# Optimization experiments

Hardware: AMD Instinct MI355X
Metric: run time of the kernel (lower is better)

The kernel has to match this reference:

```python
import jax, jax.numpy as jnp
import numpy as np

B, N, D, H = 8, 2048, 128, 128  # batch, num_nodes, input_size, hidden_size


def setup_inputs() -> dict:
    key = jax.random.key(0)
    ks = jax.random.split(key, 10)
    s = 1.0 / np.sqrt(H)
    u = lambda k, shape: jax.random.uniform(k, shape, jnp.float32, -s, s)
    return {
        "x": jax.random.normal(ks[0], (B, N, D), jnp.float32),
        "adj_matrix": jax.random.randint(ks[1], (B, N, N), 0, 2, jnp.int32),
        # PyTorch LSTM params, gate order (i, f, g, o); forward + backward dirs
        "w_ih_f": u(ks[2], (4 * H, D)),
        "w_hh_f": u(ks[3], (4 * H, H)),
        "b_ih_f": u(ks[4], (4 * H,)),
        "b_hh_f": u(ks[5], (4 * H,)),
        "w_ih_b": u(ks[6], (4 * H, D)),
        "w_hh_b": u(ks[7], (4 * H, H)),
        "b_ih_b": u(ks[8], (4 * H,)),
        "b_hh_b": u(ks[9], (4 * H,)),
    }


def _lstm_last_h(xp, w_hh):
    # xp: [T, B, 4H] precomputed input projection + biases; returns final h [B, H]
    b = xp.shape[1]
    h0 = jnp.zeros((b, H), xp.dtype)
    c0 = jnp.zeros((b, H), xp.dtype)

    def step(carry, xt):
        h, c = carry
        gates = xt + h @ w_hh.T
        i, f, g, o = jnp.split(gates, 4, axis=-1)
        c = jax.nn.sigmoid(f) * c + jax.nn.sigmoid(i) * jnp.tanh(g)
        h = jax.nn.sigmoid(o) * jnp.tanh(c)
        return (h, c), None

    (hT, _), _ = jax.lax.scan(step, (h0, c0), xp)
    return hT


def reference(x, adj_matrix, w_ih_f, w_hh_f, b_ih_f, b_hh_f, w_ih_b, w_hh_b, b_ih_b, b_hh_b):
    x = x.astype(jnp.float32)
    a = (adj_matrix > 0).astype(jnp.float32)  # [B, N, N]
    # mean over {self} + neighbors: (x_i + sum_j a_ij x_j) / (1 + deg_i)
    deg = a.sum(-1, keepdims=True)
    xa = (x + jnp.einsum('bij,bjd->bid', a, x)) / (1.0 + deg)  # [B, N, D]

    seq = jnp.swapaxes(xa, 0, 1)  # [N, B, D], time-major over nodes
    hT_f = _lstm_last_h(seq @ w_ih_f.T + (b_ih_f + b_hh_f), w_hh_f)
    hT_b = _lstm_last_h(seq[::-1] @ w_ih_b.T + (b_ih_b + b_hh_b), w_hh_b)
    return jnp.concatenate([hT_f, hT_b], axis=-1)  # [B, 2H]
```

## Files before the change

### kernel.cpp

```cpp
#include <hip/hip_runtime.h>
#include <math.h>

#define BB 8
#define NN 2048
#define DD 128
#define HH 128

typedef float f4 __attribute__((ext_vector_type(4)));
typedef __attribute__((ext_vector_type(8))) short s16x8;
typedef __attribute__((ext_vector_type(8))) unsigned short u16x8;

__device__ __forceinline__ float fast_rcp(float x) { return __builtin_amdgcn_rcpf(x); }

__device__ __forceinline__ void bsplit(float x, unsigned short& h, unsigned short& l) {
    unsigned u = __float_as_uint(x);
    unsigned r = u + 0x7FFFu + ((u >> 16) & 1u);
    h = (unsigned short)(r >> 16);
    float xh = __uint_as_float(((unsigned)h) << 16);
    float d = x - xh;
    unsigned u2 = __float_as_uint(d);
    unsigned r2 = u2 + 0x7FFFu + ((u2 >> 16) & 1u);
    l = (unsigned short)(r2 >> 16);
}

__global__ __launch_bounds__(256) void k_xT(const float* __restrict__ x,
                                            unsigned short* __restrict__ xth,
                                            unsigned short* __restrict__ xtl) {
    __shared__ __align__(16) unsigned short th[32][72];
    __shared__ __align__(16) unsigned short tl[32][72];
    const int n0 = blockIdx.x * 64;
    const int d0 = blockIdx.y * 32;
    const int b = blockIdx.z;
    const int tid = threadIdx.x;
    {
        const int nl = tid & 63, dseg = tid >> 6;
        const float* xp = x + ((size_t)b * NN + n0 + nl) * DD + d0 + dseg * 8;
        float4 v0 = *(const float4*)(xp);
        float4 v1 = *(const float4*)(xp + 4);
        const float* vv = (const float*)&v0;
#pragma unroll
        for (int j = 0; j < 4; ++j) {
            unsigned short hh, ll;
            bsplit(vv[j], hh, ll);
            th[dseg * 8 + j][nl] = hh;
            tl[dseg * 8 + j][nl] = ll;
        }
        const float* vw = (const float*)&v1;
#pragma unroll
        for (int j = 0; j < 4; ++j) {
            unsigned short hh, ll;
            bsplit(vw[j], hh, ll);
            th[dseg * 8 + 4 + j][nl] = hh;
            tl[dseg * 8 + 4 + j][nl] = ll;
        }
    }
    __syncthreads();
    {
        const int dl = tid >> 3, nseg = tid & 7;
        u16x8 vh = *(const u16x8*)&th[dl][nseg * 8];
        u16x8 vl = *(const u16x8*)&tl[dl][nseg * 8];
        size_t off = ((size_t)b * DD + d0 + dl) * NN + n0 + nseg * 8;
        *(u16x8*)(xth + off) = vh;
        *(u16x8*)(xtl + off) = vl;
    }
}

__global__ __launch_bounds__(256) void k_agg2(const int* __restrict__ adj,
                                              const unsigned short* __restrict__ xth,
                                              const unsigned short* __restrict__ xtl,
                                              unsigned short* __restrict__ xah,
                                              unsigned short* __restrict__ xal) {
    __shared__ __align__(16) unsigned short Al[64][40];
    __shared__ __align__(16) unsigned short Xh[128][40];
    __shared__ __align__(16) unsigned short Xl[128][40];
    const int b = blockIdx.y;
    const int i0 = blockIdx.x * 64;
    const int tid = threadIdx.x;
    const int wave = tid >> 6, lane = tid & 63;
    const int ar = tid >> 2, aks = (tid & 3) * 8;
    const int xd = tid >> 1, xks = (tid & 1) * 16;
    const int* ap = adj + ((size_t)b * NN + i0 + ar) * NN + aks;
    const unsigned short* hp = xth + ((size_t)b * DD + xd) * NN + xks;
    const unsigned short* lp = xtl + ((size_t)b * DD + xd) * NN + xks;

    f4 acc[8], dacc;
#pragma unroll
    for (int t = 0; t < 8; ++t) acc[t] = {0.f, 0.f, 0.f, 0.f};
    dacc = {0.f, 0.f, 0.f, 0.f};
    const short onebf = (short)0x3F80;
    s16x8 ones = {onebf, onebf, onebf, onebf, onebf, onebf, onebf, onebf};

    int4 a0 = *(const int4*)(ap);
    int4 a1 = *(const int4*)(ap + 4);
    u16x8 h0 = *(const u16x8*)(hp);
    u16x8 h1 = *(const u16x8*)(hp + 8);
    u16x8 l0 = *(const u16x8*)(lp);
    u16x8 l1 = *(const u16x8*)(lp + 8);

    for (int k0 = 0; k0 < NN; k0 += 32) {
        {
            u16x8 w;
            const int* av0 = (const int*)&a0;
            const int* av1 = (const int*)&a1;
            int colb = k0 + aks, myrow = i0 + ar;
#pragma unroll
            for (int j = 0; j < 4; ++j) {
                int c0 = (av0[j] > 0 ? 1 : 0) + (myrow == colb + j ? 1 : 0);
                int c1 = (av1[j] > 0 ? 1 : 0) + (myrow == colb + 4 + j ? 1 : 0);
                w[j] = c0 == 0 ? 0 : (c0 == 1 ? 0x3F80 : 0x4000);
                w[4 + j] = c1 == 0 ? 0 : (c1 == 1 ? 0x3F80 : 0x4000);
            }
            *(u16x8*)&Al[ar][aks] = w;
            *(u16x8*)&Xh[xd][xks] = h0;
            *(u16x8*)&Xh[xd][xks + 8] = h1;
            *(u16x8*)&Xl[xd][xks] = l0;
            *(u16x8*)&Xl[xd][xks + 8] = l1;
        }
        __syncthreads();
        if (k0 + 32 < NN) {
            a0 = *(const int4*)(ap + k0 + 32);
            a1 = *(const int4*)(ap + k0 + 36);
            h0 = *(const u16x8*)(hp + k0 + 32);
            h1 = *(const u16x8*)(hp + k0 + 40);
            l0 = *(const u16x8*)(lp + k0 + 32);
            l1 = *(const u16x8*)(lp + k0 + 40);
        }
        s16x8 afr = *(const s16x8*)&Al[16 * wave + (lane & 15)][(lane >> 4) * 8];
#pragma unroll
        for (int t = 0; t < 8; ++t) {
            s16x8 bh = *(const s16x8*)&Xh[16 * t + (lane & 15)][(lane >> 4) * 8];
            s16x8 bl = *(const s16x8*)&Xl[16 * t + (lane & 15)][(lane >> 4) * 8];
            acc[t] = __builtin_amdgcn_mfma_f32_16x16x32_bf16(afr, bh, acc[t], 0, 0, 0);
            acc[t] = __builtin_amdgcn_mfma_f32_16x16x32_bf16(afr, bl, acc[t], 0, 0, 0);
        }
        dacc = __builtin_amdgcn_mfma_f32_16x16x32_bf16(afr, ones, dacc, 0, 0, 0);
        __syncthreads();
    }
    float inv[4];
#pragma unroll
    for (int r = 0; r < 4; ++r) inv[r] = fast_rcp(dacc[r]);
#pragma unroll
    for (int t = 0; t < 8; ++t)
#pragma unroll
        for (int r = 0; r < 4; ++r) {
            int row = i0 + 16 * wave + (lane >> 4) * 4 + r;
            float v = acc[t][r] * inv[r];
            unsigned short hh, ll;
            bsplit(v, hh, ll);
            size_t base = ((size_t)b * NN + row) * DD + 16 * t + (lane & 15);
            xah[base] = hh;
            xal[base] = ll;
        }
}

__global__ __launch_bounds__(256) void k_proj2(const unsigned short* __restrict__ xah,
                                               const unsigned short* __restrict__ xal,
                                               const float* __restrict__ wif,
                                               const float* __restrict__ wib,
                                               const float* __restrict__ bif,
                                               const float* __restrict__ bhf,
                                               const float* __restrict__ bib,
                                               const float* __restrict__ bhb,
                                               float* __restrict__ xpf,
                                               float* __restrict__ xpb) {
    __shared__ __align__(16) unsigned short Wh[128][132];
    __shared__ __align__(16) unsigned short Wl[128][132];
    const int rr0 = blockIdx.x * 64;
    const int n0 = blockIdx.y * 128;
    const int tid = threadIdx.x;
    const int wave = tid >> 6, lane = tid & 63;
    {
        int g = tid >> 1;
        int d0 = (tid & 1) * 64;
        int gg = n0 + g;
        const float* wsrc = (gg < 512) ? (wif + (size_t)gg * DD) : (wib + (size_t)(gg - 512) * DD);
#pragma unroll
        for (int j = 0; j < 64; j += 4) {
            float4 v = *(const float4*)(wsrc + d0 + j);
            unsigned short hh, ll;
            bsplit(v.x, hh, ll); Wh[g][d0 + j + 0] = hh; Wl[g][d0 + j + 0] = ll;
            bsplit(v.y, hh, ll); Wh[g][d0 + j + 1] = hh; Wl[g][d0 + j + 1] = ll;
            bsplit(v.z, hh, ll); Wh[g][d0 + j + 2] = hh; Wl[g][d0 + j + 2] = ll;
            bsplit(v.w, hh, ll); Wh[g][d0 + j + 3] = hh; Wl[g][d0 + j + 3] = ll;
        }
    }
    __syncthreads();
    const int arow = rr0 + wave * 16 + (lane & 15);
    const unsigned short* ah = xah + (size_t)arow * DD + ((lane >> 4) * 8);
    const unsigned short* al = xal + (size_t)arow * DD + ((lane >> 4) * 8);
    f4 acc[8];
#pragma unroll
    for (int nt = 0; nt < 8; ++nt) acc[nt] = {0.f, 0.f, 0.f, 0.f};
#pragma unroll
    for (int k0 = 0; k0 < DD; k0 += 32) {
        s16x8 afh = *(const s16x8*)(ah + k0);
        s16x8 afl = *(const s16x8*)(al + k0);
#pragma unroll
        for (int nt = 0; nt < 8; ++nt) {
            s16x8 bh = *(const s16x8*)&Wh[nt * 16 + (lane & 15)][k0 + (lane >> 4) * 8];
            s16x8 bl = *(const s16x8*)&Wl[nt * 16 + (lane & 15)][k0 + (lane >> 4) * 8];
            acc[nt] = __builtin_amdgcn_mfma_f32_16x16x32_bf16(afh, bh, acc[nt], 0, 0, 0);
            acc[nt] = __builtin_amdgcn_mfma_f32_16x16x32_bf16(afl, bh, acc[nt], 0, 0, 0);
            acc[nt] = __builtin_amdgcn_mfma_f32_16x16x32_bf16(afh, bl, acc[nt], 0, 0, 0);
        }
    }
#pragma unroll
    for (int nt = 0; nt < 8; ++nt) {
        int gg = n0 + nt * 16 + (lane & 15);
        float bias = (gg < 512) ? (bif[gg] + bhf[gg]) : (bib[gg - 512] + bhb[gg - 512]);
#pragma unroll
        for (int r = 0; r < 4; ++r) {
            int rr = rr0 + wave * 16 + (lane >> 4) * 4 + r;
            int b = rr >> 11, t = rr & 2047;
            float v = acc[nt][r] + bias;
            if (gg < 512) {
                int pp = 4 * (gg & 127) + (gg >> 7);
                xpf[((size_t)t * BB + b) * 512 + pp] = v;
            } else {
                int gb = gg - 512;
                int pp = 4 * (gb & 127) + (gb >> 7);
                xpb[((size_t)(NN - 1 - t) * BB + b) * 512 + pp] = v;
            }
        }
    }
}


#define STRG(x) #x
#define WLD(R0, R3, WOFF, IMM)                                            \
    "global_load_dwordx4 v[" STRG(R0) ":" STRG(R3) "], %[" STRG(WOFF) "], %[whs] offset:" STRG(IMM) "\n\t"
#define PKQ(H0, H1, A0, A1, B0, B1, C0, C1, D0, D1)                                        \
    "v_pk_fma_f32 v[24:25], v[" STRG(A0) ":" STRG(A1) "], v[" STRG(H0) ":" STRG(H1) "], v[24:25]\n\t" \
    "v_pk_fma_f32 v[26:27], v[" STRG(B0) ":" STRG(B1) "], v[" STRG(H0) ":" STRG(H1) "], v[26:27]\n\t" \
    "v_pk_fma_f32 v[28:29], v[" STRG(C0) ":" STRG(C1) "], v[" STRG(H0) ":" STRG(H1) "], v[28:29]\n\t" \
    "v_pk_fma_f32 v[30:31], v[" STRG(D0) ":" STRG(D1) "], v[" STRG(H0) ":" STRG(H1) "], v[30:31]\n\t"
#define PKQ0(H0, H1, A0, A1, B0, B1, C0, C1, D0, D1)                                       \
    "v_pk_mul_f32 v[24:25], v[" STRG(A0) ":" STRG(A1) "], v[" STRG(H0) ":" STRG(H1) "]\n\t" \
    "v_pk_mul_f32 v[26:27], v[" STRG(B0) ":" STRG(B1) "], v[" STRG(H0) ":" STRG(H1) "]\n\t" \
    "v_pk_mul_f32 v[28:29], v[" STRG(C0) ":" STRG(C1) "], v[" STRG(H0) ":" STRG(H1) "]\n\t" \
    "v_pk_mul_f32 v[30:31], v[" STRG(D0) ":" STRG(D1) "], v[" STRG(H0) ":" STRG(H1) "]\n\t"

#define LSTM_BODY(XPD, XPU, RD, WR)                                                        \
    "global_load_dword " XPD ", v21, %[xps]\n\t"                                           \
    "ds_read_b128 v[32:35], " RD "\n\t"                                                    \
    "ds_read_b128 v[36:39], " RD " offset:16\n\t"                                          \
    "ds_read_b128 v[40:43], " RD " offset:32\n\t"                                          \
    "ds_read_b128 v[44:47], " RD " offset:48\n\t"                                          \
    "ds_read_b128 v[48:51], " RD " offset:64\n\t"                                          \
    "ds_read_b128 v[52:55], " RD " offset:80\n\t"                                          \
    "ds_read_b128 v[56:59], " RD " offset:96\n\t"                                          \
    "ds_read_b128 v[60:63], " RD " offset:112\n\t"                                         \
    "v_add_u32 v21, 0x4000, v21\n\t"                                                       \
    "s_waitcnt lgkmcnt(7)\n\t"                                                             \
    PKQ0(32, 33, 64, 65, 96, 97, 128, 129, 160, 161)                                       \
    PKQ(34, 35, 66, 67, 98, 99, 130, 131, 162, 163)                                        \
    "s_waitcnt lgkmcnt(6)\n\t"                                                             \
    PKQ(36, 37, 68, 69, 100, 101, 132, 133, 164, 165)                                      \
    PKQ(38, 39, 70, 71, 102, 103, 134, 135, 166, 167)                                      \
    "s_waitcnt lgkmcnt(5)\n\t"                                                             \
    PKQ(40, 41, 72, 73, 104, 105, 136, 137, 168, 169)                                      \
    PKQ(42, 43, 74, 75, 106, 107, 138, 139, 170, 171)                                      \
    "s_waitcnt lgkmcnt(4)\n\t"                                                             \
    PKQ(44, 45, 76, 77, 108, 109, 140, 141, 172, 173)                                      \
    PKQ(46, 47, 78, 79, 110, 111, 142, 143, 174, 175)                                      \
    "s_waitcnt lgkmcnt(3)\n\t"                                                             \
    PKQ(48, 49, 80, 81, 112, 113, 144, 145, 176, 177)                                      \
    PKQ(50, 51, 82, 83, 114, 115, 146, 147, 178, 179)                                      \
    "s_waitcnt lgkmcnt(2)\n\t"                                                             \
    PKQ(52, 53, 84, 85, 116, 117, 148, 149, 180, 181)                                      \
    PKQ(54, 55, 86, 87, 118, 119, 150, 151, 182, 183)                                      \
    "s_waitcnt lgkmcnt(1)\n\t"                                                             \
    PKQ(56, 57, 88, 89, 120, 121, 152, 153, 184, 185)                                      \
    PKQ(58, 59, 90, 91, 122, 123, 154, 155, 186, 187)                                      \
    "s_waitcnt lgkmcnt(0)\n\t"                                                             \
    PKQ(60, 61, 92, 93, 124, 125, 156, 157, 188, 189)                                      \
    PKQ(62, 63, 94, 95, 126, 127, 158, 159, 190, 191)                                      \
    "v_add_f32 v8, v24, v25\n\t"                                                           \
    "v_add_f32 v9, v26, v27\n\t"                                                           \
    "v_add_f32 v10, v28, v29\n\t"                                                          \
    "v_add_f32 v11, v30, v31\n\t"                                                          \
    "v_mov_b32_dpp v12, v8 quad_perm:[1,0,3,2] row_mask:0xf bank_mask:0xf\n\t"             \
    "v_mov_b32_dpp v13, v9 quad_perm:[1,0,3,2] row_mask:0xf bank_mask:0xf\n\t"             \
    "v_mov_b32_dpp v14, v10 quad_perm:[1,0,3,2] row_mask:0xf bank_mask:0xf\n\t"            \
    "v_mov_b32_dpp v15, v11 quad_perm:[1,0,3,2] row_mask:0xf bank_mask:0xf\n\t"            \
    "v_add_f32 v8, v8, v12\n\t"                                                            \
    "v_add_f32 v9, v9, v13\n\t"                                                            \
    "v_add_f32 v10, v10, v14\n\t"                                                          \
    "v_add_f32 v11, v11, v15\n\t"                                                          \
    "v_mov_b32_dpp v12, v8 quad_perm:[2,3,0,1] row_mask:0xf bank_mask:0xf\n\t"             \
    "v_mov_b32_dpp v13, v9 quad_perm:[2,3,0,1] row_mask:0xf bank_mask:0xf\n\t"             \
    "v_mov_b32_dpp v14, v10 quad_perm:[2,3,0,1] row_mask:0xf bank_mask:0xf\n\t"            \
    "v_mov_b32_dpp v15, v11 quad_perm:[2,3,0,1] row_mask:0xf bank_mask:0xf\n\t"            \
    "v_add_f32 v8, v8, v12\n\t"                                                            \
    "v_add_f32 v9, v9, v13\n\t"                                                            \
    "v_add_f32 v10, v10, v14\n\t"                                                          \
    "v_add_f32 v11, v11, v15\n\t"                                                          \
    "v_mul_f32 v12, %[s0], v8\n\t"                                                         \
    "v_fma_f32 v12, %[s1], v9, v12\n\t"                                                    \
    "v_fma_f32 v12, %[s2], v10, v12\n\t"                                                   \
    "s_waitcnt vmcnt(1)\n\t"                                                               \
    "v_fma_f32 v12, %[s3], v11, v12\n\t"                                                   \
    "v_add_f32 v12, v12, " XPU "\n\t"                                                      \
    "v_mul_f32 v13, %[ml], v12\n\t"                                                        \
    "v_exp_f32 v13, v13\n\t"                                                               \
    "s_nop 1\n\t"                                                                          \
    "v_add_f32 v13, 1.0, v13\n\t"                                                          \
    "v_rcp_f32 v13, v13\n\t"                                                               \
    "s_nop 1\n\t"                                                                          \
    "v_fma_f32 v12, %[Aa], v13, %[Ba]\n\t"                                                 \
    "s_nop 1\n\t"                                                                          \
    "v_mov_b32_dpp v13, v12 quad_perm:[0,0,0,0] row_mask:0xf bank_mask:0xf\n\t"            \
    "v_mov_b32_dpp v14, v12 quad_perm:[2,2,2,2] row_mask:0xf bank_mask:0xf\n\t"            \
    "v_mov_b32_dpp v15, v12 quad_perm:[1,1,1,1] row_mask:0xf bank_mask:0xf\n\t"            \
    "v_mov_b32_dpp v17, v12 quad_perm:[3,3,3,3] row_mask:0xf bank_mask:0xf\n\t"            \
    "v_mul_f32 v13, v13, v14\n\t"                                                          \
    "v_fma_f32 v16, v15, v16, v13\n\t"                                                     \
    "v_mul_f32 v14, 0xc038aa3b, v16\n\t"                                                   \
    "v_exp_f32 v14, v14\n\t"                                                               \
    "s_nop 1\n\t"                                                                          \
    "v_add_f32 v14, 1.0, v14\n\t"                                                          \
    "v_rcp_f32 v14, v14\n\t"                                                               \
    "s_nop 1\n\t"                                                                          \
    "v_fma_f32 v14, 2.0, v14, -1.0\n\t"                                                    \
    "v_mul_f32 v17, v14, v17\n\t"                                                          \
    "ds_write_b32 " WR ", v17\n\t"                                                         \
    "s_waitcnt lgkmcnt(0)\n\t"                                                             \
    "s_barrier\n\t"

__global__ __launch_bounds__(512) void k_lstm(const float* __restrict__ xpf,
                                              const float* __restrict__ xpb,
                                              const float* __restrict__ whf,
                                              const float* __restrict__ whb,
                                              float* __restrict__ out) {
    const int b = blockIdx.x;
    const int dir = blockIdx.y;
    const float* __restrict__ xp = dir ? xpb : xpf;
    const float* __restrict__ wh = dir ? whb : whf;
    const int t = threadIdx.x;
    const int q = t >> 2;
    const int jq = t & 3;

    __shared__ __align__(64) float h_lds[1088];
    for (int i = t; i < 1088; i += 512) h_lds[i] = 0.f;
    __syncthreads();

    unsigned hbase = (unsigned)(uintptr_t)&h_lds[0];
    unsigned rd0 = hbase + 672u * (unsigned)jq;
    unsigned rd1 = rd0 + 2176u;
    unsigned wrE = hbase + 2176u + 544u * (unsigned)jq + ((unsigned)q << 2);
    unsigned wrO = wrE - 2176u;
    unsigned w0 = ((0u * 128u + (unsigned)q) * 128u + (unsigned)jq * 32u) * 4u;
    unsigned w1 = ((1u * 128u + (unsigned)q) * 128u + (unsigned)jq * 32u) * 4u;
    unsigned w2 = ((2u * 128u + (unsigned)q) * 128u + (unsigned)jq * 32u) * 4u;
    unsigned w3 = ((3u * 128u + (unsigned)q) * 128u + (unsigned)jq * 32u) * 4u;
    unsigned xoff = (unsigned)(b * 512 + t) * 4u + 16384u;
    float xp0v = xp[(size_t)b * 512 + t];
    float s0 = (jq == 0) ? 1.f : 0.f;
    float s1 = (jq == 1) ? 1.f : 0.f;
    float s2 = (jq == 2) ? 1.f : 0.f;
    float s3 = (jq == 3) ? 1.f : 0.f;
    float mlv = (jq == 2) ? -2.8853900817779268f : -1.4426950408889634f;
    float Aav = (jq == 2) ? 2.f : 1.f;
    float Bav = (jq == 2) ? -1.f : 0.f;
    float h_out;

    asm volatile(
        "v_mov_b32 v16, 0\n\t"
        "s_movk_i32 s20, 0x400\n\t"
        "v_mov_b32 v19, %[x0]\n\t"
        "v_mov_b32 v21, %[xo]\n\t"
        "v_mov_b32 v22, %[rdb]\n\t"
        "v_mov_b32 v18, %[rdb2]\n\t"
        "v_mov_b32 v23, %[wrb]\n\t"
        "v_mov_b32 v192, %[wrb2]\n\t"
        WLD(64, 67, w0, 0) WLD(68, 71, w0, 16) WLD(72, 75, w0, 32) WLD(76, 79, w0, 48)
        WLD(80, 83, w0, 64) WLD(84, 87, w0, 80) WLD(88, 91, w0, 96) WLD(92, 95, w0, 112)
        WLD(96, 99, w1, 0) WLD(100, 103, w1, 16) WLD(104, 107, w1, 32) WLD(108, 111, w1, 48)
        WLD(112, 115, w1, 64) WLD(116, 119, w1, 80) WLD(120, 123, w1, 96) WLD(124, 127, w1, 112)
        WLD(128, 131, w2, 0) WLD(132, 135, w2, 16) WLD(136, 139, w2, 32) WLD(140, 143, w2, 48)
        WLD(144, 147, w2, 64) WLD(148, 151, w2, 80) WLD(152, 155, w2, 96) WLD(156, 159, w2, 112)
        WLD(160, 163, w3, 0) WLD(164, 167, w3, 16) WLD(168, 171, w3, 32) WLD(172, 175, w3, 48)
        WLD(176, 179, w3, 64) WLD(180, 183, w3, 80) WLD(184, 187, w3, 96) WLD(188, 191, w3, 112)
        "s_waitcnt vmcnt(0)\n\t"
        "LSTM_TOP%=:\n\t"
        LSTM_BODY("v20", "v19", "v22", "v23")
        LSTM_BODY("v19", "v20", "v18", "v192")
        "s_sub_u32 s20, s20, 1\n\t"
        "s_cmp_lg_u32 s20, 0\n\t"
        "s_cbranch_scc1 LSTM_TOP%=\n\t"
        "v_mov_b32 %[ho], v17\n\t"
        : [ho] "=v"(h_out)
        : [w0] "v"(w0), [w1] "v"(w1), [w2] "v"(w2), [w3] "v"(w3),
          [whs] "s"(wh), [xps] "s"(xp),
          [xo] "v"(xoff), [rdb] "v"(rd0), [rdb2] "v"(rd1),
          [wrb] "v"(wrE), [wrb2] "v"(wrO), [x0] "v"(xp0v),
          [s0] "v"(s0), [s1] "v"(s1), [s2] "v"(s2), [s3] "v"(s3),
          [ml] "v"(mlv), [Aa] "v"(Aav), [Ba] "v"(Bav)
        : "memory", "vcc", "scc", "s20",
          "v8", "v9", "v10", "v11", "v12", "v13", "v14", "v15", "v16", "v17",
          "v18", "v19", "v20", "v21", "v22", "v23", "v24", "v25", "v26", "v27",
          "v28", "v29", "v30", "v31", "v32", "v33", "v34", "v35", "v36", "v37",
          "v38", "v39", "v40", "v41", "v42", "v43", "v44", "v45", "v46", "v47",
          "v48", "v49", "v50", "v51", "v52", "v53", "v54", "v55", "v56", "v57",
          "v58", "v59", "v60", "v61", "v62", "v63", "v64", "v65", "v66", "v67",
          "v68", "v69", "v70", "v71", "v72", "v73", "v74", "v75", "v76", "v77",
          "v78", "v79", "v80", "v81", "v82", "v83", "v84", "v85", "v86", "v87",
          "v88", "v89", "v90", "v91", "v92", "v93", "v94", "v95", "v96", "v97",
          "v98", "v99", "v100", "v101", "v102", "v103", "v104", "v105", "v106", "v107",
          "v108", "v109", "v110", "v111", "v112", "v113", "v114", "v115", "v116", "v117",
          "v118", "v119", "v120", "v121", "v122", "v123", "v124", "v125", "v126", "v127",
          "v128", "v129", "v130", "v131", "v132", "v133", "v134", "v135", "v136", "v137",
          "v138", "v139", "v140", "v141", "v142", "v143", "v144", "v145", "v146", "v147",
          "v148", "v149", "v150", "v151", "v152", "v153", "v154", "v155", "v156", "v157",
          "v158", "v159", "v160", "v161", "v162", "v163", "v164", "v165", "v166", "v167",
          "v168", "v169", "v170", "v171", "v172", "v173", "v174", "v175", "v176", "v177",
          "v178", "v179", "v180", "v181", "v182", "v183", "v184", "v185", "v186", "v187",
          "v188", "v189", "v190", "v191", "v192");

    if (jq == 0) out[(size_t)b * 256 + dir * HH + q] = h_out;
}

extern "C" void kernel_launch(void* const* d_in, const int* in_sizes, int n_in,
                              void* d_out, int out_size, void* d_ws, size_t ws_size,
                              hipStream_t stream) {
    const float* x = (const float*)d_in[0];
    const int* adj = (const int*)d_in[1];
    const float* wif = (const float*)d_in[2];
    const float* whf = (const float*)d_in[3];
    const float* bif = (const float*)d_in[4];
    const float* bhf = (const float*)d_in[5];
    const float* wib = (const float*)d_in[6];
    const float* whb = (const float*)d_in[7];
    const float* bib = (const float*)d_in[8];
    const float* bhb = (const float*)d_in[9];
    float* out = (float*)d_out;

    float* xpf = (float*)d_ws;
    float* xpb = xpf + (size_t)NN * BB * 512;
    unsigned short* xah = (unsigned short*)(xpb + (size_t)NN * BB * 512);
    unsigned short* xal = xah + (size_t)BB * NN * DD;
    unsigned short* xth = (unsigned short*)xpf;
    unsigned short* xtl = xth + (size_t)BB * DD * NN;

    k_xT<<<dim3(NN / 64, DD / 32, BB), 256, 0, stream>>>(x, xth, xtl);
    k_agg2<<<dim3(NN / 64, BB), 256, 0, stream>>>(adj, xth, xtl, xah, xal);
    k_proj2<<<dim3((NN * BB) / 64, 1024 / 128), 256, 0, stream>>>(xah, xal, wif, wib, bif, bhf,
                                                                  bib, bhb, xpf, xpb);
    k_lstm<<<dim3(BB, 2), 512, 0, stream>>>(xpf, xpb, whf, whb, out);
}
```

Measured before the change: 1.209 ms.

## Split aggregation tile across eight waves by row and column halves

```diff
diff --git a/kernel.cpp b/kernel.cpp
--- a/kernel.cpp
+++ b/kernel.cpp
@@ -9,6 +9,7 @@
 typedef float f4 __attribute__((ext_vector_type(4)));
 typedef __attribute__((ext_vector_type(8))) short s16x8;
 typedef __attribute__((ext_vector_type(8))) unsigned short u16x8;
+typedef __attribute__((ext_vector_type(4))) unsigned short u16x4;
 
 __device__ __forceinline__ float fast_rcp(float x) { return __builtin_amdgcn_rcpf(x); }
 
@@ -65,7 +66,7 @@
     }
 }
 
-__global__ __launch_bounds__(256) void k_agg2(const int* __restrict__ adj,
+__global__ __launch_bounds__(512) void k_agg2(const int* __restrict__ adj,
                                               const unsigned short* __restrict__ xth,
                                               const unsigned short* __restrict__ xtl,
                                               unsigned short* __restrict__ xah,
@@ -77,59 +78,50 @@
     const int i0 = blockIdx.x * 64;
     const int tid = threadIdx.x;
     const int wave = tid >> 6, lane = tid & 63;
-    const int ar = tid >> 2, aks = (tid & 3) * 8;
-    const int xd = tid >> 1, xks = (tid & 1) * 16;
-    const int* ap = adj + ((size_t)b * NN + i0 + ar) * NN + aks;
+    const int rt = wave >> 1;
+    const int colh = wave & 1;
+    const int ar = tid >> 3, ak = (tid & 7) * 4;
+    const int xd = tid >> 2, xks = (tid & 3) * 8;
+    const int* ap = adj + ((size_t)b * NN + i0 + ar) * NN + ak;
     const unsigned short* hp = xth + ((size_t)b * DD + xd) * NN + xks;
     const unsigned short* lp = xtl + ((size_t)b * DD + xd) * NN + xks;
 
-    f4 acc[8], dacc;
-#pragma unroll
-    for (int t = 0; t < 8; ++t) acc[t] = {0.f, 0.f, 0.f, 0.f};
+    f4 acc[4], dacc;
+#pragma unroll
+    for (int t = 0; t < 4; ++t) acc[t] = {0.f, 0.f, 0.f, 0.f};
     dacc = {0.f, 0.f, 0.f, 0.f};
     const short onebf = (short)0x3F80;
     s16x8 ones = {onebf, onebf, onebf, onebf, onebf, onebf, onebf, onebf};
 
     int4 a0 = *(const int4*)(ap);
-    int4 a1 = *(const int4*)(ap + 4);
     u16x8 h0 = *(const u16x8*)(hp);
-    u16x8 h1 = *(const u16x8*)(hp + 8);
     u16x8 l0 = *(const u16x8*)(lp);
-    u16x8 l1 = *(const u16x8*)(lp + 8);
 
     for (int k0 = 0; k0 < NN; k0 += 32) {
         {
-            u16x8 w;
-            const int* av0 = (const int*)&a0;
-            const int* av1 = (const int*)&a1;
-            int colb = k0 + aks, myrow = i0 + ar;
+            u16x4 w;
+            const int* av = (const int*)&a0;
+            int colb = k0 + ak, myrow = i0 + ar;
 #pragma unroll
             for (int j = 0; j < 4; ++j) {
-                int c0 = (av0[j] > 0 ? 1 : 0) + (myrow == colb + j ? 1 : 0);
-                int c1 = (av1[j] > 0 ? 1 : 0) + (myrow == colb + 4 + j ? 1 : 0);
-                w[j] = c0 == 0 ? 0 : (c0 == 1 ? 0x3F80 : 0x4000);
-                w[4 + j] = c1 == 0 ? 0 : (c1 == 1 ? 0x3F80 : 0x4000);
+                int c = (av[j] > 0 ? 1 : 0) + (myrow == colb + j ? 1 : 0);
+                w[j] = c == 0 ? 0 : (c == 1 ? 0x3F80 : 0x4000);
             }
-            *(u16x8*)&Al[ar][aks] = w;
+            *(u16x4*)&Al[ar][ak] = w;
             *(u16x8*)&Xh[xd][xks] = h0;
-            *(u16x8*)&Xh[xd][xks + 8] = h1;
             *(u16x8*)&Xl[xd][xks] = l0;
-            *(u16x8*)&Xl[xd][xks + 8] = l1;
         }
         __syncthreads();
         if (k0 + 32 < NN) {
             a0 = *(const int4*)(ap + k0 + 32);
-            a1 = *(const int4*)(ap + k0 + 36);
             h0 = *(const u16x8*)(hp + k0 + 32);
-            h1 = *(const u16x8*)(hp + k0 + 40);
             l0 = *(const u16x8*)(lp + k0 + 32);
-            l1 = *(const u16x8*)(lp + k0 + 40);
-        }
-        s16x8 afr = *(const s16x8*)&Al[16 * wave + (lane & 15)][(lane >> 4) * 8];
-#pragma unroll
-        for (int t = 0; t < 8; ++t) {
-            s16x8 bh = *(const s16x8*)&Xh[16 * t + (lane & 15)][(lane >> 4) * 8];
-            s16x8 bl = *(const s16x8*)&Xl[16 * t + (lane & 15)][(lane >> 4) * 8];
+        }
+        s16x8 afr = *(const s16x8*)&Al[rt * 16 + (lane & 15)][(lane >> 4) * 8];
+#pragma unroll
+        for (int t = 0; t < 4; ++t) {
+            s16x8 bh = *(const s16x8*)&Xh[colh * 64 + 16 * t + (lane & 15)][(lane >> 4) * 8];
+            s16x8 bl = *(const s16x8*)&Xl[colh * 64 + 16 * t + (lane & 15)][(lane >> 4) * 8];
             acc[t] = __builtin_amdgcn_mfma_f32_16x16x32_bf16(afr, bh, acc[t], 0, 0, 0);
             acc[t] = __builtin_amdgcn_mfma_f32_16x16x32_bf16(afr, bl, acc[t], 0, 0, 0);
         }
@@ -140,14 +132,15 @@
 #pragma unroll
     for (int r = 0; r < 4; ++r) inv[r] = fast_rcp(dacc[r]);
 #pragma unroll
-    for (int t = 0; t < 8; ++t)
+    for (int t = 0; t < 4; ++t)
 #pragma unroll
         for (int r = 0; r < 4; ++r) {
-            int row = i0 + 16 * wave + (lane >> 4) * 4 + r;
+            int row = i0 + rt * 16 + (lane >> 4) * 4 + r;
+            int col = colh * 64 + 16 * t + (lane & 15);
             float v = acc[t][r] * inv[r];
             unsigned short hh, ll;
             bsplit(v, hh, ll);
-            size_t base = ((size_t)b * NN + row) * DD + 16 * t + (lane & 15);
+            size_t base = ((size_t)b * NN + row) * DD + col;
             xah[base] = hh;
             xal[base] = ll;
         }
@@ -443,7 +436,7 @@
     unsigned short* xtl = xth + (size_t)BB * DD * NN;
 
     k_xT<<<dim3(NN / 64, DD / 32, BB), 256, 0, stream>>>(x, xth, xtl);
-    k_agg2<<<dim3(NN / 64, BB), 256, 0, stream>>>(adj, xth, xtl, xah, xal);
+    k_agg2<<<dim3(NN / 64, BB), 512, 0, stream>>>(adj, xth, xtl, xah, xal);
     k_proj2<<<dim3((NN * BB) / 64, 1024 / 128), 256, 0, stream>>>(xah, xal, wif, wib, bif, bhf,
                                                                   bib, bhb, xpf, xpb);
     k_lstm<<<dim3(BB, 2), 512, 0, stream>>>(xpf, xpb, whf, whb, out);
```

After: 1.205 ms. Within noise of the previous version (-0.3%).
